# Kernel optimization log

Measured on AMD Instinct MI355X. Metric: run time of the kernel, lower is better.

The kernel has to match this reference:

```python
import jax, jax.numpy as jnp
import numpy as np
import math

B, L = 2, 512
D_MODEL = 64
N_HEAD = 8
N_GLOBAL = 64
N_ITER = 2
DISTS = 4
K_RANK = 4
REG_H = 1.0
REG_Z = 1.0
NEG = -1e9


def setup_inputs() -> dict:
    key = jax.random.key(0)
    k1, k2, k3, k4 = jax.random.split(key, 4)
    x = jax.random.normal(k1, (B, L, D_MODEL), dtype=jnp.float32)
    mask = jnp.ones((B, L), dtype=jnp.int32)
    # nn.init.normal_ defaults (std=1)
    distribution_params = jax.random.normal(k2, (2 * DISTS, K_RANK), dtype=jnp.float32)
    ternary = jax.random.normal(k3, (K_RANK, D_MODEL, D_MODEL, N_HEAD), dtype=jnp.float32)
    # global_: std = 1/sqrt(d_model), single-channel -> heads dim = 1
    global_param = jax.random.normal(k4, (N_GLOBAL, D_MODEL, 1), dtype=jnp.float32) * (1.0 / math.sqrt(D_MODEL))
    return {"x": x, "mask": mask, "distribution_params": distribution_params,
            "ternary": ternary, "global_param": global_param}


def _softmax(s):
    return jax.nn.softmax(s, axis=-1)


def _distmask(distribution_params, n, dtype):
    # distance(i,j) = clip(i - j, -dists, dists); row 0 of params is zeros (distance 0)
    dist = jnp.arange(n)[:, None] - jnp.arange(n)[None, :]
    dist = jnp.clip(dist, -DISTS, DISTS)
    params = jnp.concatenate([jnp.zeros((1, K_RANK), dtype), distribution_params], axis=0)  # [2*dists+1, k]
    # torch negative indexing wraps; emulate explicitly
    idx = jnp.where(dist < 0, dist + 2 * DISTS + 1, dist)
    return params[idx].transpose(2, 0, 1)  # [k, n, n]


def reference(x, mask, distribution_params, ternary, global_param):
    bsz, n, d = x.shape
    mask1d = mask != 0                                   # [B, L]
    mask2d = mask1d[:, :, None] & mask1d[:, None, :]     # [B, L, L]
    inv2d = ~mask2d[:, None, :, :]                       # [B, 1, L, L] broadcast over heads
    inv1d = ~mask1d[:, None, :, None]                    # [B, 1, L, 1]

    distmask = _distmask(distribution_params, n, x.dtype)  # [k, L, L]

    unary = x
    q_z = unary
    for _ in range(N_ITER):
        # --- normalize Z beliefs (softmax over d_model states) ---
        Q_z = _softmax(q_z / REG_Z)                      # [B, L, d]
        # precompute decomposed tensor messages: M1[z,k,j,a,c] = sum_b Qz[z,j,b] T[k,a,b,c]
        M1 = jnp.einsum('zjb,kabc->zkjac', Q_z, ternary)  # [B, k, L, d, h]
        # --- H update (each head of token i picks a parent j) ---
        # s_h[z,c,i,j] = sum_{a,k} Qz[z,i,a] M1[z,k,j,a,c] distmask[k,i,j]
        s_h = jnp.einsum('zia,zkjac,kij->zcij', Q_z, M1, distmask)  # [B, h, L, L]
        s_h = jnp.where(inv2d, NEG, s_h)
        Q_h = _softmax(s_h / REG_H)                      # softmax over parents j
        # --- global H update (single channel): token i picks one of n_global global nodes ---
        s_g = jnp.einsum('zia,gac->zcig', Q_z, global_param)        # [B, 1, L, G]
        s_g = jnp.where(inv1d, NEG, s_g)
        Q_g = _softmax(s_g / REG_H)
        # --- Z update: messages from ternary factors in both roles + global factor ---
        g1 = jnp.einsum('zcij,zkjac,kij->zia', Q_h, M1, distmask)   # token as Z_i
        M2 = jnp.einsum('zjb,kbac->zkjac', Q_z, ternary)            # swapped roles
        g2 = jnp.einsum('zcji,zkjac,kji->zia', Q_h, M2, distmask)   # token as Z_j
        gg = jnp.einsum('zcig,gac->zia', Q_g, global_param)         # global message
        q_z = unary + g1 + g2 + gg
        # damping=0, stepsize=1 -> plain full update
    # output_prob=False -> unnormalized scores
    return q_z
```

## Files before the change

### kernel.cpp

```cpp
#include <hip/hip_runtime.h>

#define BB 2
#define LL 512
#define DD 64
#define HH 8
#define GG 64
#define KK 4
#define NEGV -1e9f
#define NSLOT 36

typedef unsigned short ushort_t;
typedef __attribute__((ext_vector_type(8))) short bf16x8;
typedef __attribute__((ext_vector_type(4))) float f32x4;
#define MFMA(a, b, c) __builtin_amdgcn_mfma_f32_16x16x32_bf16(a, b, c, 0, 0, 0)

__device__ __forceinline__ ushort_t f2b(float f) {
    unsigned int u = __float_as_uint(f);
    return (ushort_t)((u + 0x7FFFu + ((u >> 16) & 1u)) >> 16);
}
__device__ __forceinline__ float b2f(ushort_t s) {
    return __uint_as_float(((unsigned int)s) << 16);
}

__device__ __forceinline__ void stage64(ushort_t* dst, const ushort_t* src,
                                        int rowstride, int tid) {
#pragma unroll
    for (int g = tid; g < 512; g += 256) {
        int row = g >> 3, colg = g & 7;
        uint4 v = *reinterpret_cast<const uint4*>(&src[row * rowstride + (colg << 3)]);
        *reinterpret_cast<uint4*>(&dst[(row << 6) + ((colg ^ (row & 7)) << 3)]) = v;
    }
}
__device__ __forceinline__ bf16x8 frag(const ushort_t* s, int row, int col) {
    return *reinterpret_cast<const bf16x8*>(&s[(row << 6) + ((((col >> 3) ^ (row & 7))) << 3)]);
}
__device__ __forceinline__ bf16x8 maskfrag(bf16x8 v, int cnt, bool keep_prefix) {
    bf16x8 r;
#pragma unroll
    for (int u = 0; u < 8; ++u) {
        bool keep = keep_prefix ? (u < cnt) : (u >= cnt);
        r[u] = keep ? v[u] : (short)0;
    }
    return r;
}
__device__ __forceinline__ int iclamp(int v, int lo, int hi) {
    return v < lo ? lo : (v > hi ? hi : v);
}

__global__ __launch_bounds__(256) void k_prepT(const float* __restrict__ T,
                                               ushort_t* __restrict__ TB1,
                                               ushort_t* __restrict__ TB2) {
    int k = blockIdx.x >> 3, c = blockIdx.x & 7;
    int tid = threadIdx.x;
    for (int g = tid; g < 512; g += 256) {
        int a = g >> 3, b0 = (g & 7) * 8;
        ushort_t o1[8], o2[8];
#pragma unroll
        for (int u = 0; u < 8; ++u) {
            o1[u] = f2b(T[(((k * 64 + a) * 64) + b0 + u) * 8 + c]);
            o2[u] = f2b(T[(((k * 64 + b0 + u) * 64) + a) * 8 + c]);
        }
        size_t base = ((size_t)(k * 8 + c) * 64 + a) * 64 + b0;
        *reinterpret_cast<uint4*>(&TB1[base]) = *reinterpret_cast<uint4*>(o1);
        *reinterpret_cast<uint4*>(&TB2[base]) = *reinterpret_cast<uint4*>(o2);
    }
}

__global__ __launch_bounds__(256) void k_softmax_qz(const float* __restrict__ src,
                                                    float* __restrict__ Qz,
                                                    ushort_t* __restrict__ QzB) {
    int row = blockIdx.x * 4 + (threadIdx.x >> 6);
    int lane = threadIdx.x & 63;
    float v = src[row * DD + lane];
    float m = v;
#pragma unroll
    for (int o = 32; o > 0; o >>= 1) m = fmaxf(m, __shfl_xor(m, o, 64));
    float e = __expf(v - m);
    float s = e;
#pragma unroll
    for (int o = 32; o > 0; o >>= 1) s += __shfl_xor(s, o, 64);
    float r = e / s;
    Qz[row * DD + lane] = r;
    QzB[row * DD + lane] = f2b(r);
}

__global__ __launch_bounds__(256) void k_compute_M(const ushort_t* __restrict__ QzB,
        const ushort_t* __restrict__ TB1, const ushort_t* __restrict__ TB2,
        ushort_t* __restrict__ M1Nb, ushort_t* __restrict__ M2Nb) {
    int jt = blockIdx.x, c = blockIdx.y;
    int z = blockIdx.z >> 2, k = blockIdx.z & 3;
    __shared__ ushort_t sQ[4096], sB1[4096], sB2[4096];
    int tid = threadIdx.x;
    stage64(sQ, QzB + (size_t)(z * LL + jt * 64) * DD, DD, tid);
    size_t tb = (size_t)(k * 8 + c) * 4096;
    stage64(sB1, TB1 + tb, 64, tid);
    stage64(sB2, TB2 + tb, 64, tid);
    __syncthreads();
    int w = tid >> 6, lm = tid & 15, lg = (tid & 63) >> 4;
    f32x4 a1[4], a2[4];
#pragma unroll
    for (int nf = 0; nf < 4; ++nf) { a1[nf] = {0.f,0.f,0.f,0.f}; a2[nf] = {0.f,0.f,0.f,0.f}; }
#pragma unroll
    for (int ks = 0; ks < 2; ++ks) {
        int kc = ks * 32 + lg * 8;
        bf16x8 af = frag(sQ, w * 16 + lm, kc);
#pragma unroll
        for (int nf = 0; nf < 4; ++nf) {
            a1[nf] = MFMA(af, frag(sB1, nf * 16 + lm, kc), a1[nf]);
            a2[nf] = MFMA(af, frag(sB2, nf * 16 + lm, kc), a2[nf]);
        }
    }
    size_t base = (((size_t)z * KK + k) * HH + c) * LL;
#pragma unroll
    for (int nf = 0; nf < 4; ++nf)
#pragma unroll
        for (int r = 0; r < 4; ++r) {
            int j = jt * 64 + w * 16 + lg * 4 + r;
            int a = nf * 16 + lm;
            M1Nb[(base + j) * DD + a] = f2b(a1[nf][r]);
            M2Nb[(base + j) * DD + a] = f2b(a2[nf][r]);
        }
}

__global__ __launch_bounds__(256, 4) void k_collaux(const float* __restrict__ Qz,
        const ushort_t* __restrict__ M1Nb, const ushort_t* __restrict__ M2Nb,
        const float* __restrict__ dp, const float* __restrict__ gp, const int* __restrict__ mask,
        ushort_t* __restrict__ MPNb, ushort_t* __restrict__ MMNb,
        ushort_t* __restrict__ MP2Nb, ushort_t* __restrict__ MM2Nb,
        ushort_t* __restrict__ MPT, ushort_t* __restrict__ MMT,
        ushort_t* __restrict__ MP2T, ushort_t* __restrict__ MM2T,
        float* __restrict__ BAND, float* __restrict__ QG) {
    __shared__ __align__(16) ushort_t sT[4 * 64 * 65];
    int tid = threadIdx.x;
    int b = blockIdx.x;
    if (b < 128) {
        int jt = b & 7, zc = b >> 3;
        int z = zc >> 3, c = zc & 7;
        ushort_t* sP1 = sT;
        ushort_t* sM1 = sT + 64 * 65;
        ushort_t* sP2 = sT + 2 * 64 * 65;
        ushort_t* sM2 = sT + 3 * 64 * 65;
        float w4[4], w5[4];
#pragma unroll
        for (int k = 0; k < 4; ++k) { w4[k] = dp[12 + k]; w5[k] = dp[16 + k]; }
        size_t b0 = (((size_t)z * KK * HH + c) * LL + jt * 64) * DD;
        const size_t kstr = (size_t)HH * LL * DD;
        for (int g = tid; g < 512; g += 256) {
            int j = g >> 3, a0 = (g & 7) * 8;
            size_t o = b0 + (size_t)j * DD + a0;
            float p1[8] = {}, q1[8] = {}, p2[8] = {}, q2[8] = {};
#pragma unroll
            for (int k = 0; k < 4; ++k) {
                uint4 v1 = *reinterpret_cast<const uint4*>(&M1Nb[o + k * kstr]);
                uint4 v2 = *reinterpret_cast<const uint4*>(&M2Nb[o + k * kstr]);
                const ushort_t* s1 = reinterpret_cast<const ushort_t*>(&v1);
                const ushort_t* s2 = reinterpret_cast<const ushort_t*>(&v2);
#pragma unroll
                for (int u = 0; u < 8; ++u) {
                    float f1 = b2f(s1[u]), f2v = b2f(s2[u]);
                    p1[u] += w4[k] * f1; q1[u] += w5[k] * f1;
                    p2[u] += w4[k] * f2v; q2[u] += w5[k] * f2v;
                }
            }
            ushort_t t1[8], t2[8], t3[8], t4[8];
#pragma unroll
            for (int u = 0; u < 8; ++u) {
                t1[u] = f2b(p1[u]); t2[u] = f2b(q1[u]); t3[u] = f2b(p2[u]); t4[u] = f2b(q2[u]);
                sP1[(a0 + u) * 65 + j] = t1[u]; sM1[(a0 + u) * 65 + j] = t2[u];
                sP2[(a0 + u) * 65 + j] = t3[u]; sM2[(a0 + u) * 65 + j] = t4[u];
            }
            size_t on = ((size_t)zc * LL + jt * 64 + j) * DD + a0;
            *reinterpret_cast<uint4*>(&MPNb[on])  = *reinterpret_cast<uint4*>(t1);
            *reinterpret_cast<uint4*>(&MMNb[on])  = *reinterpret_cast<uint4*>(t2);
            *reinterpret_cast<uint4*>(&MP2Nb[on]) = *reinterpret_cast<uint4*>(t3);
            *reinterpret_cast<uint4*>(&MM2Nb[on]) = *reinterpret_cast<uint4*>(t4);
        }
        __syncthreads();
        for (int g = tid; g < 512; g += 256) {
            int a = g >> 3, j0 = (g & 7) * 8;
            ushort_t o1[8], o2[8], o3[8], o4[8];
#pragma unroll
            for (int u = 0; u < 8; ++u) {
                o1[u] = sP1[a * 65 + j0 + u]; o2[u] = sM1[a * 65 + j0 + u];
                o3[u] = sP2[a * 65 + j0 + u]; o4[u] = sM2[a * 65 + j0 + u];
            }
            size_t ot = ((size_t)zc * DD + a) * LL + jt * 64 + j0;
            *reinterpret_cast<uint4*>(&MPT[ot])  = *reinterpret_cast<uint4*>(o1);
            *reinterpret_cast<uint4*>(&MMT[ot])  = *reinterpret_cast<uint4*>(o2);
            *reinterpret_cast<uint4*>(&MP2T[ot]) = *reinterpret_cast<uint4*>(o3);
            *reinterpret_cast<uint4*>(&MM2T[ot]) = *reinterpret_cast<uint4*>(o4);
        }
    } else if (b < 2176) {
        int w = (b - 128) * 4 + (tid >> 6);
        int lane = tid & 63;
        int j = w & 511, c = (w >> 9) & 7, z = w >> 12;
        float m[4];
#pragma unroll
        for (int k = 0; k < 4; ++k)
            m[k] = b2f(M1Nb[((((size_t)z * KK + k) * HH + c) * LL + j) * DD + lane]);
        float out = 0.f;
#pragma unroll
        for (int d = -3; d <= 3; ++d) {
            int i = j + d;
            if (i < 0 || i >= LL) continue;
            int idx = d < 0 ? d + 9 : d;
            float t = 0.f;
            if (idx != 0) {
#pragma unroll
                for (int k = 0; k < 4; ++k) t += dp[(idx - 1) * 4 + k] * m[k];
            }
            float s = Qz[(z * LL + i) * DD + lane] * t;
#pragma unroll
            for (int o = 32; o > 0; o >>= 1) s += __shfl_xor(s, o, 64);
            if (lane == d + 3) out = s;
        }
        if (lane < 7) BAND[(size_t)w * 8 + lane] = out;
    } else {
        float* gpS = reinterpret_cast<float*>(sT);
#pragma unroll
        for (int idx = tid; idx < 4096; idx += 256) gpS[(idx >> 6) * 68 + (idx & 63)] = gp[idx];
        __syncthreads();
        int row = (b - 2176) * 4 + (tid >> 6);
        int g = tid & 63;
        float qv = Qz[row * DD + g];
        float s = 0.f;
#pragma unroll 8
        for (int a = 0; a < 64; ++a) s += __shfl(qv, a, 64) * gpS[g * 68 + a];
        if (mask[row] == 0) s = NEGV;
        float m = s;
#pragma unroll
        for (int o = 32; o > 0; o >>= 1) m = fmaxf(m, __shfl_xor(m, o, 64));
        float e = __expf(s - m);
        float sum = e;
#pragma unroll
        for (int o = 32; o > 0; o >>= 1) sum += __shfl_xor(sum, o, 64);
        QG[row * GG + g] = e / sum;
    }
}

__global__ __launch_bounds__(256, 4) void k_sh(const ushort_t* __restrict__ QzB,
        const ushort_t* __restrict__ MPNb, const ushort_t* __restrict__ MMNb,
        const float* __restrict__ BAND, const int* __restrict__ mask,
        float* __restrict__ SH) {
    int jt = blockIdx.x, it = blockIdx.y;
    int z = blockIdx.z >> 3, c = blockIdx.z & 7;
    __shared__ ushort_t sA[4096], sB[4096];
    int tid = threadIdx.x;
    stage64(sA, QzB + ((size_t)(z * LL + it * 64)) * DD, DD, tid);
    bool diag = (it == jt);
    size_t bbase = ((size_t)(z * HH + c) * LL + jt * 64) * DD;
    const ushort_t* B0 = diag ? MPNb : (it > jt ? MPNb : MMNb);
    stage64(sB, B0 + bbase, DD, tid);
    __syncthreads();
    int w = tid >> 6, lm = tid & 15, lg = (tid & 63) >> 4;
    f32x4 accP[4], accM[4];
#pragma unroll
    for (int nf = 0; nf < 4; ++nf) { accP[nf] = {0.f,0.f,0.f,0.f}; accM[nf] = {0.f,0.f,0.f,0.f}; }
#pragma unroll
    for (int ks = 0; ks < 2; ++ks) {
        int kc = ks * 32 + lg * 8;
        bf16x8 af = frag(sA, w * 16 + lm, kc);
#pragma unroll
        for (int nf = 0; nf < 4; ++nf)
            accP[nf] = MFMA(af, frag(sB, nf * 16 + lm, kc), accP[nf]);
    }
    if (diag) {
        __syncthreads();
        stage64(sB, MMNb + bbase, DD, tid);
        __syncthreads();
#pragma unroll
        for (int ks = 0; ks < 2; ++ks) {
            int kc = ks * 32 + lg * 8;
            bf16x8 af = frag(sA, w * 16 + lm, kc);
#pragma unroll
            for (int nf = 0; nf < 4; ++nf)
                accM[nf] = MFMA(af, frag(sB, nf * 16 + lm, kc), accM[nf]);
        }
    }
    int mi[4];
#pragma unroll
    for (int r = 0; r < 4; ++r) mi[r] = mask[z * LL + it * 64 + w * 16 + lg * 4 + r];
#pragma unroll
    for (int nf = 0; nf < 4; ++nf) {
        int j = jt * 64 + nf * 16 + lm;
        int mjv = mask[z * LL + j];
#pragma unroll
        for (int r = 0; r < 4; ++r) {
            int i = it * 64 + w * 16 + lg * 4 + r;
            float v = (diag && i <= j) ? accM[nf][r] : accP[nf][r];
            int d = i - j;
            if (d >= -3 && d <= 3)
                v = BAND[((size_t)((z * HH + c) * LL + j)) * 8 + (d + 3)];
            if (!(mi[r] && mjv)) v = NEGV;
            SH[((size_t)(z * HH + c) * LL + i) * LL + j] = v;
        }
    }
}

__global__ __launch_bounds__(256) void k_softmax_sh(const float* __restrict__ SH,
                                                    ushort_t* __restrict__ SHB) {
    int row = blockIdx.x * 4 + (threadIdx.x >> 6);
    int lane = threadIdx.x & 63;
    float v[8];
    float m = -1e30f;
#pragma unroll
    for (int r = 0; r < 8; ++r) { v[r] = SH[(size_t)row * LL + r * 64 + lane]; m = fmaxf(m, v[r]); }
#pragma unroll
    for (int o = 32; o > 0; o >>= 1) m = fmaxf(m, __shfl_xor(m, o, 64));
    float s = 0.f;
#pragma unroll
    for (int r = 0; r < 8; ++r) { v[r] = __expf(v[r] - m); s += v[r]; }
#pragma unroll
    for (int o = 32; o > 0; o >>= 1) s += __shfl_xor(s, o, 64);
    float inv = 1.f / s;
#pragma unroll
    for (int r = 0; r < 8; ++r)
        SHB[(size_t)row * LL + r * 64 + lane] = f2b(v[r] * inv);
}

__global__ __launch_bounds__(256) void k_transp(const ushort_t* __restrict__ SHB,
                                                ushort_t* __restrict__ SHBT) {
    int it = blockIdx.x, jt = blockIdx.y, zc = blockIdx.z;
    __shared__ ushort_t t[64][72];
    int tid = threadIdx.x;
#pragma unroll
    for (int g = tid; g < 512; g += 256) {
        int jj = g >> 3, cg = g & 7;
        uint4 v = *reinterpret_cast<const uint4*>(
            &SHB[((size_t)zc * LL + jt * 64 + jj) * LL + it * 64 + cg * 8]);
        *reinterpret_cast<uint4*>(&t[jj][cg * 8]) = v;
    }
    __syncthreads();
#pragma unroll
    for (int g = tid; g < 512; g += 256) {
        int ii = g >> 3, cg = g & 7;
        ushort_t tmp[8];
#pragma unroll
        for (int u = 0; u < 8; ++u) tmp[u] = t[cg * 8 + u][ii];
        *reinterpret_cast<uint4*>(
            &SHBT[((size_t)zc * LL + it * 64 + ii) * LL + jt * 64 + cg * 8]) =
            *reinterpret_cast<uint4*>(tmp);
    }
}

__global__ __launch_bounds__(256, 4) void k_g12corr(const ushort_t* __restrict__ SHB,
        const ushort_t* __restrict__ SHBT,
        const ushort_t* __restrict__ MPT, const ushort_t* __restrict__ MMT,
        const ushort_t* __restrict__ MP2T, const ushort_t* __restrict__ MM2T,
        const ushort_t* __restrict__ M1Nb, const ushort_t* __restrict__ M2Nb,
        const ushort_t* __restrict__ MPNb, const ushort_t* __restrict__ MMNb,
        const ushort_t* __restrict__ MP2Nb, const ushort_t* __restrict__ MM2Nb,
        const float* __restrict__ dp, float* __restrict__ PG) {
    __shared__ ushort_t sSH[4096], sM[4096];
    int tid = threadIdx.x;
    int b = blockIdx.x;
    if (b < 512) {
        int it = b & 7, jc = (b >> 3) & 1, zcw = b >> 4;
        int which = zcw >> 4;
        int z = (zcw >> 3) & 1, c = zcw & 7;
        const ushort_t* Amat = which ? SHBT : SHB;
        const ushort_t* TP = which ? MP2T : MPT;
        const ushort_t* TM = which ? MM2T : MMT;
        int w = tid >> 6, lm = tid & 15, lg = (tid & 63) >> 4;
        f32x4 acc[4];
#pragma unroll
        for (int nf = 0; nf < 4; ++nf) acc[nf] = {0.f,0.f,0.f,0.f};
        size_t shbase = ((size_t)(z * HH + c) * LL + it * 64) * LL;
        size_t mbase  = ((size_t)(z * HH + c) * DD) * LL;
        for (int js = 0; js < 4; ++js) {
            int j0 = jc * 256 + js * 64;
            bool dg = (j0 == it * 64);
            bool useP = which == 0 ? (j0 < it * 64) : (j0 > it * 64);
            __syncthreads();
            stage64(sSH, Amat + shbase + j0, LL, tid);
            stage64(sM, (dg ? TP : (useP ? TP : TM)) + mbase + j0, LL, tid);
            __syncthreads();
            for (int pass = 0; pass < (dg ? 2 : 1); ++pass) {
                if (pass == 1) {
                    __syncthreads();
                    stage64(sM, TM + mbase + j0, LL, tid);
                    __syncthreads();
                }
#pragma unroll
                for (int ks = 0; ks < 2; ++ks) {
                    int kc = ks * 32 + lg * 8;
                    int jb = j0 + kc;
                    bf16x8 af = frag(sSH, w * 16 + lm, kc);
                    if (dg) {
                        int i = it * 64 + w * 16 + lm;
                        int cnt = (which == 0) ? iclamp(i - jb, 0, 8) : iclamp(i + 1 - jb, 0, 8);
                        af = maskfrag(af, cnt, (pass == 0) == (which == 0));
                    }
#pragma unroll
                    for (int nf = 0; nf < 4; ++nf)
                        acc[nf] = MFMA(af, frag(sM, nf * 16 + lm, kc), acc[nf]);
                }
            }
        }
        int slot = which * 16 + c * 2 + jc;
#pragma unroll
        for (int nf = 0; nf < 4; ++nf)
#pragma unroll
            for (int r = 0; r < 4; ++r) {
                int i = it * 64 + w * 16 + lg * 4 + r;
                int a = nf * 16 + lm;
                PG[((size_t)(slot * BB + z) * LL + i) * DD + a] = acc[nf][r];
            }
    } else {
        int bid = b - 512;
        int which = bid >> 9; bid &= 511;
        int w = bid * 4 + (tid >> 6);
        int lane = tid & 63;
        int ch = w & 1, i = (w >> 1) & 511, z = w >> 10;
        const ushort_t* Mx = which ? M2Nb : M1Nb;
        const ushort_t* MPb = which ? MP2Nb : MPNb;
        const ushort_t* MMb = which ? MM2Nb : MMNb;
        float acc = 0.f;
        for (int cc = 0; cc < 4; ++cc) {
            int c = ch * 4 + cc;
#pragma unroll
            for (int d = -3; d <= 3; ++d) {
                int j = which ? i + d : i - d;
                if (j < 0 || j >= LL) continue;
                float qh = which ? b2f(SHB[(((size_t)z * HH + c) * LL + j) * LL + i])
                                 : b2f(SHB[(((size_t)z * HH + c) * LL + i) * LL + j]);
                int idx = d < 0 ? d + 9 : d;
                float e = 0.f;
                if (idx != 0) {
#pragma unroll
                    for (int k = 0; k < 4; ++k)
                        e += dp[(idx - 1) * 4 + k] *
                             b2f(Mx[((((size_t)z * KK + k) * HH + c) * LL + j) * DD + lane]);
                }
                const ushort_t* mb = (d > 0) ? MPb : MMb;
                float mn = b2f(mb[(((size_t)z * HH + c) * LL + j) * DD + lane]);
                acc += qh * (e - mn);
            }
        }
        int slot = 32 + which * 2 + ch;
        PG[(((size_t)slot * BB + z) * LL + i) * DD + lane] = acc;
    }
}

__global__ __launch_bounds__(256) void k_update(const float* __restrict__ x, const float* __restrict__ PG,
                         const float* __restrict__ QG, const float* __restrict__ gp,
                         float* __restrict__ outq) {
    __shared__ __align__(16) float gpS[64][68];
    int tid = threadIdx.x;
#pragma unroll
    for (int idx = tid; idx < 4096; idx += 256) gpS[idx >> 6][idx & 63] = gp[idx];
    __syncthreads();
    int row = blockIdx.x * 4 + (tid >> 6);
    int a = tid & 63;
    float acc = x[row * DD + a];
    float qgv = QG[row * GG + a];
#pragma unroll 8
    for (int g = 0; g < 64; ++g) acc += __shfl(qgv, g, 64) * gpS[g][a];
#pragma unroll 6
    for (int s = 0; s < NSLOT; ++s) acc += PG[((size_t)s * BB * LL + row) * DD + a];
    outq[row * DD + a] = acc;
}

extern "C" void kernel_launch(void* const* d_in, const int* in_sizes, int n_in,
                              void* d_out, int out_size, void* d_ws, size_t ws_size,
                              hipStream_t stream) {
    const float* x    = (const float*)d_in[0];
    const int*   mask = (const int*)d_in[1];
    const float* dp   = (const float*)d_in[2];
    const float* T    = (const float*)d_in[3];
    const float* gp   = (const float*)d_in[4];
    float* out = (float*)d_out;

    float* p = (float*)d_ws;
    float* Qz = p;                        p += 65536;
    ushort_t* QzB = (ushort_t*)p;         p += 32768;
    ushort_t* TB1 = (ushort_t*)p;         p += 65536;
    ushort_t* TB2 = (ushort_t*)p;         p += 65536;
    ushort_t* M1Nb = (ushort_t*)p;        p += 1048576;
    ushort_t* M2Nb = (ushort_t*)p;        p += 1048576;
    ushort_t* MPNb  = (ushort_t*)p;       p += 262144;
    ushort_t* MMNb  = (ushort_t*)p;       p += 262144;
    ushort_t* MP2Nb = (ushort_t*)p;       p += 262144;
    ushort_t* MM2Nb = (ushort_t*)p;       p += 262144;
    ushort_t* MPT   = (ushort_t*)p;       p += 262144;
    ushort_t* MMT   = (ushort_t*)p;       p += 262144;
    ushort_t* MP2T  = (ushort_t*)p;       p += 262144;
    ushort_t* MM2T  = (ushort_t*)p;       p += 262144;
    float* BAND = p;                      p += 65536;
    float* SH   = p;                      p += 4194304;
    ushort_t* SHB  = (ushort_t*)p;        p += 2097152;
    ushort_t* SHBT = (ushort_t*)p;        p += 2097152;
    float* QG   = p;                      p += 65536;
    float* PG   = p;                      p += (size_t)NSLOT * 65536;
    float* QZ1  = p;                      p += 65536;

    hipLaunchKernelGGL(k_prepT, dim3(32), dim3(256), 0, stream, T, TB1, TB2);

    const float* qsrc = x;
    for (int iter = 0; iter < 2; ++iter) {
        float* qdst = (iter == 0) ? QZ1 : out;
        hipLaunchKernelGGL(k_softmax_qz, dim3(256), dim3(256), 0, stream, qsrc, Qz, QzB);
        hipLaunchKernelGGL(k_compute_M, dim3(8, 8, 8), dim3(256), 0, stream, QzB, TB1, TB2, M1Nb, M2Nb);
        hipLaunchKernelGGL(k_collaux, dim3(2432), dim3(256), 0, stream, Qz, M1Nb, M2Nb, dp, gp, mask,
                           MPNb, MMNb, MP2Nb, MM2Nb, MPT, MMT, MP2T, MM2T, BAND, QG);
        hipLaunchKernelGGL(k_sh, dim3(8, 8, 16), dim3(256), 0, stream, QzB, MPNb, MMNb, BAND, mask, SH);
        hipLaunchKernelGGL(k_softmax_sh, dim3(2048), dim3(256), 0, stream, SH, SHB);
        hipLaunchKernelGGL(k_transp, dim3(8, 8, 16), dim3(256), 0, stream, SHB, SHBT);
        hipLaunchKernelGGL(k_g12corr, dim3(1536), dim3(256), 0, stream, SHB, SHBT,
                           MPT, MMT, MP2T, MM2T, M1Nb, M2Nb,
                           MPNb, MMNb, MP2Nb, MM2Nb, dp, PG);
        hipLaunchKernelGGL(k_update, dim3(256), dim3(256), 0, stream, x, PG, QG, gp, qdst);
        qsrc = qdst;
    }
}
```

Baseline: 150.1 us.

## Fuse score GEMM, row softmax and transpose into one kernel

Three kernels (score computation writing fp32 SH, row softmax to bf16, and tile transpose) are merged into one kernel. Each block now handles a full 64-row strip across all 512 columns, keeps the scores in registers, does the softmax with cross-lane shuffles, and writes both SHB and its transpose SHBT through a shared-memory tile. This removes the fp32 SH round trip and two launches. In exchange the grid shrinks to 128 blocks with 128 accumulator floats per thread, which lowers occupancy and parallelism.

```diff
diff --git a/kernel.cpp b/kernel.cpp
--- a/kernel.cpp
+++ b/kernel.cpp
@@ -238,35 +238,29 @@
     }
 }
 
-__global__ __launch_bounds__(256, 4) void k_sh(const ushort_t* __restrict__ QzB,
+__global__ __launch_bounds__(256, 2) void k_shsm(const ushort_t* __restrict__ QzB,
         const ushort_t* __restrict__ MPNb, const ushort_t* __restrict__ MMNb,
         const float* __restrict__ BAND, const int* __restrict__ mask,
-        float* __restrict__ SH) {
-    int jt = blockIdx.x, it = blockIdx.y;
-    int z = blockIdx.z >> 3, c = blockIdx.z & 7;
+        ushort_t* __restrict__ SHB, ushort_t* __restrict__ SHBT) {
+    int it = blockIdx.x, zc = blockIdx.y;
+    int z = zc >> 3;
     __shared__ ushort_t sA[4096], sB[4096];
+    __shared__ ushort_t tl[64 * 72];
     int tid = threadIdx.x;
-    stage64(sA, QzB + ((size_t)(z * LL + it * 64)) * DD, DD, tid);
-    bool diag = (it == jt);
-    size_t bbase = ((size_t)(z * HH + c) * LL + jt * 64) * DD;
-    const ushort_t* B0 = diag ? MPNb : (it > jt ? MPNb : MMNb);
-    stage64(sB, B0 + bbase, DD, tid);
-    __syncthreads();
     int w = tid >> 6, lm = tid & 15, lg = (tid & 63) >> 4;
-    f32x4 accP[4], accM[4];
-#pragma unroll
-    for (int nf = 0; nf < 4; ++nf) { accP[nf] = {0.f,0.f,0.f,0.f}; accM[nf] = {0.f,0.f,0.f,0.f}; }
-#pragma unroll
-    for (int ks = 0; ks < 2; ++ks) {
-        int kc = ks * 32 + lg * 8;
-        bf16x8 af = frag(sA, w * 16 + lm, kc);
-#pragma unroll
-        for (int nf = 0; nf < 4; ++nf)
-            accP[nf] = MFMA(af, frag(sB, nf * 16 + lm, kc), accP[nf]);
-    }
-    if (diag) {
+    stage64(sA, QzB + (size_t)(z * LL + it * 64) * DD, DD, tid);
+    f32x4 acc[8][4];
+#pragma unroll
+    for (int jt = 0; jt < 8; ++jt)
+#pragma unroll
+        for (int nf = 0; nf < 4; ++nf) acc[jt][nf] = {0.f, 0.f, 0.f, 0.f};
+#pragma unroll
+    for (int jt = 0; jt < 8; ++jt) {
+        bool diag = (it == jt);
+        size_t bbase = ((size_t)zc * LL + jt * 64) * DD;
+        const ushort_t* B0 = diag ? MPNb : (it > jt ? MPNb : MMNb);
         __syncthreads();
-        stage64(sB, MMNb + bbase, DD, tid);
+        stage64(sB, B0 + bbase, DD, tid);
         __syncthreads();
 #pragma unroll
         for (int ks = 0; ks < 2; ++ks) {
@@ -274,72 +268,100 @@
             bf16x8 af = frag(sA, w * 16 + lm, kc);
 #pragma unroll
             for (int nf = 0; nf < 4; ++nf)
-                accM[nf] = MFMA(af, frag(sB, nf * 16 + lm, kc), accM[nf]);
+                acc[jt][nf] = MFMA(af, frag(sB, nf * 16 + lm, kc), acc[jt][nf]);
+        }
+        if (diag) {
+            __syncthreads();
+            stage64(sB, MMNb + bbase, DD, tid);
+            __syncthreads();
+            f32x4 accM[4];
+#pragma unroll
+            for (int nf = 0; nf < 4; ++nf) accM[nf] = {0.f, 0.f, 0.f, 0.f};
+#pragma unroll
+            for (int ks = 0; ks < 2; ++ks) {
+                int kc = ks * 32 + lg * 8;
+                bf16x8 af = frag(sA, w * 16 + lm, kc);
+#pragma unroll
+                for (int nf = 0; nf < 4; ++nf)
+                    accM[nf] = MFMA(af, frag(sB, nf * 16 + lm, kc), accM[nf]);
+            }
+#pragma unroll
+            for (int nf = 0; nf < 4; ++nf)
+#pragma unroll
+                for (int r = 0; r < 4; ++r) {
+                    int i = it * 64 + w * 16 + lg * 4 + r;
+                    int j = jt * 64 + nf * 16 + lm;
+                    if (i <= j) acc[jt][nf][r] = accM[nf][r];
+                }
         }
     }
     int mi[4];
 #pragma unroll
     for (int r = 0; r < 4; ++r) mi[r] = mask[z * LL + it * 64 + w * 16 + lg * 4 + r];
 #pragma unroll
-    for (int nf = 0; nf < 4; ++nf) {
-        int j = jt * 64 + nf * 16 + lm;
-        int mjv = mask[z * LL + j];
-#pragma unroll
-        for (int r = 0; r < 4; ++r) {
-            int i = it * 64 + w * 16 + lg * 4 + r;
-            float v = (diag && i <= j) ? accM[nf][r] : accP[nf][r];
-            int d = i - j;
-            if (d >= -3 && d <= 3)
-                v = BAND[((size_t)((z * HH + c) * LL + j)) * 8 + (d + 3)];
-            if (!(mi[r] && mjv)) v = NEGV;
-            SH[((size_t)(z * HH + c) * LL + i) * LL + j] = v;
-        }
-    }
-}
-
-__global__ __launch_bounds__(256) void k_softmax_sh(const float* __restrict__ SH,
-                                                    ushort_t* __restrict__ SHB) {
-    int row = blockIdx.x * 4 + (threadIdx.x >> 6);
-    int lane = threadIdx.x & 63;
-    float v[8];
-    float m = -1e30f;
-#pragma unroll
-    for (int r = 0; r < 8; ++r) { v[r] = SH[(size_t)row * LL + r * 64 + lane]; m = fmaxf(m, v[r]); }
-#pragma unroll
-    for (int o = 32; o > 0; o >>= 1) m = fmaxf(m, __shfl_xor(m, o, 64));
-    float s = 0.f;
-#pragma unroll
-    for (int r = 0; r < 8; ++r) { v[r] = __expf(v[r] - m); s += v[r]; }
-#pragma unroll
-    for (int o = 32; o > 0; o >>= 1) s += __shfl_xor(s, o, 64);
-    float inv = 1.f / s;
-#pragma unroll
-    for (int r = 0; r < 8; ++r)
-        SHB[(size_t)row * LL + r * 64 + lane] = f2b(v[r] * inv);
-}
-
-__global__ __launch_bounds__(256) void k_transp(const ushort_t* __restrict__ SHB,
-                                                ushort_t* __restrict__ SHBT) {
-    int it = blockIdx.x, jt = blockIdx.y, zc = blockIdx.z;
-    __shared__ ushort_t t[64][72];
-    int tid = threadIdx.x;
-#pragma unroll
-    for (int g = tid; g < 512; g += 256) {
-        int jj = g >> 3, cg = g & 7;
-        uint4 v = *reinterpret_cast<const uint4*>(
-            &SHB[((size_t)zc * LL + jt * 64 + jj) * LL + it * 64 + cg * 8]);
-        *reinterpret_cast<uint4*>(&t[jj][cg * 8]) = v;
-    }
-    __syncthreads();
-#pragma unroll
-    for (int g = tid; g < 512; g += 256) {
-        int ii = g >> 3, cg = g & 7;
-        ushort_t tmp[8];
-#pragma unroll
-        for (int u = 0; u < 8; ++u) tmp[u] = t[cg * 8 + u][ii];
-        *reinterpret_cast<uint4*>(
-            &SHBT[((size_t)zc * LL + it * 64 + ii) * LL + jt * 64 + cg * 8]) =
-            *reinterpret_cast<uint4*>(tmp);
+    for (int jt = 0; jt < 8; ++jt) {
+#pragma unroll
+        for (int nf = 0; nf < 4; ++nf) {
+            int j = jt * 64 + nf * 16 + lm;
+            int mjv = mask[z * LL + j];
+#pragma unroll
+            for (int r = 0; r < 4; ++r) {
+                int i = it * 64 + w * 16 + lg * 4 + r;
+                int d = i - j;
+                float v = acc[jt][nf][r];
+                if (d >= -3 && d <= 3) v = BAND[((size_t)zc * LL + j) * 8 + (d + 3)];
+                if (!(mi[r] && mjv)) v = NEGV;
+                acc[jt][nf][r] = v;
+            }
+        }
+    }
+    float inv[4];
+#pragma unroll
+    for (int r = 0; r < 4; ++r) {
+        float m = -1e30f;
+#pragma unroll
+        for (int jt = 0; jt < 8; ++jt)
+#pragma unroll
+            for (int nf = 0; nf < 4; ++nf) m = fmaxf(m, acc[jt][nf][r]);
+#pragma unroll
+        for (int o = 1; o < 16; o <<= 1) m = fmaxf(m, __shfl_xor(m, o, 64));
+        float s = 0.f;
+#pragma unroll
+        for (int jt = 0; jt < 8; ++jt)
+#pragma unroll
+            for (int nf = 0; nf < 4; ++nf) {
+                float e = __expf(acc[jt][nf][r] - m);
+                acc[jt][nf][r] = e;
+                s += e;
+            }
+#pragma unroll
+        for (int o = 1; o < 16; o <<= 1) s += __shfl_xor(s, o, 64);
+        inv[r] = 1.f / s;
+    }
+#pragma unroll
+    for (int jt = 0; jt < 8; ++jt) {
+        __syncthreads();
+#pragma unroll
+        for (int nf = 0; nf < 4; ++nf)
+#pragma unroll
+            for (int r = 0; r < 4; ++r)
+                tl[(w * 16 + lg * 4 + r) * 72 + nf * 16 + lm] = f2b(acc[jt][nf][r] * inv[r]);
+        __syncthreads();
+        for (int g = tid; g < 512; g += 256) {
+            int row = g >> 3, c0 = (g & 7) * 8;
+            ushort_t tmp[8];
+#pragma unroll
+            for (int u = 0; u < 8; ++u) tmp[u] = tl[row * 72 + c0 + u];
+            *reinterpret_cast<uint4*>(
+                &SHB[((size_t)zc * LL + it * 64 + row) * LL + jt * 64 + c0]) =
+                *reinterpret_cast<uint4*>(tmp);
+            ushort_t tmp2[8];
+#pragma unroll
+            for (int u = 0; u < 8; ++u) tmp2[u] = tl[(c0 + u) * 72 + row];
+            *reinterpret_cast<uint4*>(
+                &SHBT[((size_t)zc * LL + jt * 64 + row) * LL + it * 64 + c0]) =
+                *reinterpret_cast<uint4*>(tmp2);
+        }
     }
 }
 
@@ -487,7 +509,6 @@
     ushort_t* MP2T  = (ushort_t*)p;       p += 262144;
     ushort_t* MM2T  = (ushort_t*)p;       p += 262144;
     float* BAND = p;                      p += 65536;
-    float* SH   = p;                      p += 4194304;
     ushort_t* SHB  = (ushort_t*)p;        p += 2097152;
     ushort_t* SHBT = (ushort_t*)p;        p += 2097152;
     float* QG   = p;                      p += 65536;
@@ -503,9 +524,8 @@
         hipLaunchKernelGGL(k_compute_M, dim3(8, 8, 8), dim3(256), 0, stream, QzB, TB1, TB2, M1Nb, M2Nb);
         hipLaunchKernelGGL(k_collaux, dim3(2432), dim3(256), 0, stream, Qz, M1Nb, M2Nb, dp, gp, mask,
                            MPNb, MMNb, MP2Nb, MM2Nb, MPT, MMT, MP2T, MM2T, BAND, QG);
-        hipLaunchKernelGGL(k_sh, dim3(8, 8, 16), dim3(256), 0, stream, QzB, MPNb, MMNb, BAND, mask, SH);
-        hipLaunchKernelGGL(k_softmax_sh, dim3(2048), dim3(256), 0, stream, SH, SHB);
-        hipLaunchKernelGGL(k_transp, dim3(8, 8, 16), dim3(256), 0, stream, SHB, SHBT);
+        hipLaunchKernelGGL(k_shsm, dim3(8, 16), dim3(256), 0, stream, QzB, MPNb, MMNb, BAND, mask,
+                           SHB, SHBT);
         hipLaunchKernelGGL(k_g12corr, dim3(1536), dim3(256), 0, stream, SHB, SHBT,
                            MPT, MMT, MP2T, MM2T, M1Nb, M2Nb,
                            MPNb, MMNb, MP2Nb, MM2Nb, dp, PG);
```

Result: slower. 158.8 us (+5.8%).
